# Performance work log

Measured on AMD Instinct MI355X. Metric: run time of the kernel, lower is better.

Reference implementation:

```python
import jax, jax.numpy as jnp
import numpy as np

N_NODES = 50000
N_EDGES = 800000
IN_DIM = 768
HID = 32
HEADS = 4
OUT_DIM = 128


def setup_inputs() -> dict:
    key = jax.random.key(0)
    ks = jax.random.split(key, 7)
    h = jax.random.normal(ks[0], (N_NODES, IN_DIM), dtype=jnp.float32)
    W1 = jax.random.normal(ks[1], (HEADS, IN_DIM, HID), dtype=jnp.float32) * (1.0 / np.sqrt(IN_DIM))
    a1 = jax.random.normal(ks[2], (HEADS, 2 * HID), dtype=jnp.float32) * (1.0 / np.sqrt(2 * HID))
    W2 = jax.random.normal(ks[3], (1, HEADS * HID, OUT_DIM), dtype=jnp.float32) * (1.0 / np.sqrt(HEADS * HID))
    a2 = jax.random.normal(ks[4], (1, 2 * OUT_DIM), dtype=jnp.float32) * (1.0 / np.sqrt(2 * OUT_DIM))
    src = jax.random.randint(ks[5], (N_EDGES,), 0, N_NODES, dtype=jnp.int32)
    dst = jax.random.randint(ks[6], (N_EDGES,), 0, N_NODES, dtype=jnp.int32)
    return {"h": h, "W1": W1, "a1": a1, "W2": W2, "a2": a2, "src": src, "dst": dst}


def gat_layer(h, W, a, src, dst, n_nodes):
    # W: [H, Din, D], a: [H, 2D]; returns concat of heads: [N, H*D]
    z = jnp.einsum('ni,hio->nho', h, W)          # [N, H, D]
    D = z.shape[-1]
    a_src, a_dst = a[:, :D], a[:, D:]
    s_src = jnp.einsum('nhd,hd->nh', z, a_src)   # [N, H]
    s_dst = jnp.einsum('nhd,hd->nh', z, a_dst)
    e = jax.nn.leaky_relu(s_src[src] + s_dst[dst], 0.01)  # [E, H]
    # edge softmax over incoming edges of each dst node
    e_max = jax.ops.segment_max(e, dst, num_segments=n_nodes)
    e_max = jnp.where(jnp.isfinite(e_max), e_max, 0.0)     # empty segments -> -inf
    ex = jnp.exp(e - e_max[dst])
    denom = jax.ops.segment_sum(ex, dst, num_segments=n_nodes)
    alpha = ex / jnp.maximum(denom[dst], 1e-9)             # [E, H]
    msg = alpha[:, :, None] * z[src]                       # [E, H, D]
    out = jax.ops.segment_sum(msg, dst, num_segments=n_nodes)  # [N, H, D]
    return out.reshape(n_nodes, -1)


def reference(h, W1, a1, W2, a2, src, dst):
    n = h.shape[0]
    h1 = jax.nn.elu(gat_layer(h, W1, a1, src, dst, n))   # [N, HEADS*HID]
    h2 = gat_layer(h1, W2, a2, src, dst, n)              # [N, OUT_DIM]
    return h2
```

## Files before the change

### kernel.cpp

```cpp
#include <hip/hip_runtime.h>

#define NN 50000
#define NE 800000
#define IND 768
#define CH  128
#define NBLK 196
#define GBM 64
#define GBK 32
#define MBLKS 782

typedef __attribute__((ext_vector_type(8))) short bf16x8;
typedef __attribute__((ext_vector_type(4))) float f32x4;

__device__ __forceinline__ unsigned short bf16_rne(float f) {
    unsigned u = __float_as_uint(f);
    u += 0x7fffu + ((u >> 16) & 1u);
    return (unsigned short)(u >> 16);
}
__device__ __forceinline__ float bf16_to_f(unsigned short b) {
    return __uint_as_float(((unsigned)b) << 16);
}

__global__ void prep_b1(const float* __restrict__ W1,
                        unsigned short* __restrict__ Bhi, unsigned short* __restrict__ Blo)
{
    int idx = blockIdx.x * blockDim.x + threadIdx.x;
    if (idx >= CH * IND) return;
    int n = idx / IND, k = idx % IND;
    float v = W1[(size_t)(n >> 5) * IND * 32 + (size_t)k * 32 + (n & 31)];
    int kt = k >> 5, kk = k & 31, j = kk >> 3, e = kk & 7;
    int g = n * 4 + (j ^ ((n >> 1) & 3));
    int off = kt * 4096 + g * 8 + e;
    unsigned short hi = bf16_rne(v);
    float lo = v - bf16_to_f(hi);
    Bhi[off] = hi;
    Blo[off] = bf16_rne(lo);
}

__global__ void prep_b2(const float* __restrict__ W2,
                        unsigned short* __restrict__ Bhi, unsigned short* __restrict__ Blo)
{
    int idx = blockIdx.x * blockDim.x + threadIdx.x;
    if (idx >= CH * CH) return;
    int n = idx / CH, k = idx % CH;
    float v = W2[(size_t)k * CH + n];
    int kt = k >> 5, kk = k & 31, j = kk >> 3, e = kk & 7;
    int g = n * 4 + (j ^ ((n >> 1) & 3));
    int off = kt * 4096 + g * 8 + e;
    unsigned short hi = bf16_rne(v);
    float lo = v - bf16_to_f(hi);
    Bhi[off] = hi;
    Blo[off] = bf16_rne(lo);
}

template<int H>
__global__ __launch_bounds__(256) void gemm_fused(
    const float* __restrict__ A,
    const unsigned short* __restrict__ Bthi, const unsigned short* __restrict__ Btlo,
    const float* __restrict__ av,
    unsigned short* __restrict__ Z16,
    float* __restrict__ ss, float* __restrict__ sd, int K)
{
    __shared__ unsigned short Ahi[2048];
    __shared__ unsigned short Alo[2048];
    __shared__ unsigned short Bs[2][4096];
    __shared__ float sred[2][64][2];

    const int t = threadIdx.x;
    const int lane = t & 63;
    const int w = t >> 6;
    const int wr = w >> 1, wc = w & 1;
    const int lrow = lane & 15, kg = lane >> 4;
    const int m0 = blockIdx.x * GBM;
    const int nt = K >> 5;

    const int ar = t >> 2, aj = t & 3;
    const bool avalid = (m0 + ar) < NN;
    const float* aptr = A + (size_t)(avalid ? (m0 + ar) : 0) * K + aj * 8;
    const int ag8 = (ar * 4 + (aj ^ ((ar >> 1) & 3))) * 8;

    int aoff[2];
    #pragma unroll
    for (int mi = 0; mi < 2; ++mi) {
        const int r = wr * 32 + mi * 16 + lrow;
        aoff[mi] = (r * 4 + (kg ^ ((r >> 1) & 3))) * 8;
    }
    int boff[4];
    #pragma unroll
    for (int ni = 0; ni < 4; ++ni) {
        const int n = wc * 64 + ni * 16 + lrow;
        boff[ni] = (n * 4 + (kg ^ ((n >> 1) & 3))) * 8;
    }

    f32x4 acc[2][4];
    #pragma unroll
    for (int i = 0; i < 2; ++i)
        #pragma unroll
        for (int j = 0; j < 4; ++j) acc[i][j] = (f32x4)(0.f);

    for (int kt = 0; kt < nt; ++kt) {
        float4 v0 = make_float4(0.f, 0.f, 0.f, 0.f);
        float4 v1 = make_float4(0.f, 0.f, 0.f, 0.f);
        if (avalid) {
            const float* p = aptr + kt * GBK;
            v0 = *(const float4*)p;
            v1 = *(const float4*)(p + 4);
        }
        float f[8] = {v0.x, v0.y, v0.z, v0.w, v1.x, v1.y, v1.z, v1.w};
        unsigned short hi[8], lo[8];
        #pragma unroll
        for (int q = 0; q < 8; ++q) {
            hi[q] = bf16_rne(f[q]);
            lo[q] = bf16_rne(f[q] - bf16_to_f(hi[q]));
        }
        __syncthreads();
        *(uint4*)&Ahi[ag8] = *(uint4*)hi;
        *(uint4*)&Alo[ag8] = *(uint4*)lo;
        #pragma unroll
        for (int i = 0; i < 4; ++i) {
            const int c = w * 4 + i;
            const int plane = c >> 3;
            const int co = (c & 7) * 512;
            const unsigned short* gs =
                (plane ? Btlo : Bthi) + (size_t)kt * 4096 + co + lane * 8;
            __builtin_amdgcn_global_load_lds(
                (const __attribute__((address_space(1))) unsigned int*)gs,
                (__attribute__((address_space(3))) unsigned int*)&Bs[plane][co],
                16, 0, 0);
        }
        __syncthreads();

        bf16x8 ahi[2], alo[2];
        #pragma unroll
        for (int mi = 0; mi < 2; ++mi) {
            ahi[mi] = *(const bf16x8*)&Ahi[aoff[mi]];
            alo[mi] = *(const bf16x8*)&Alo[aoff[mi]];
        }
        #pragma unroll
        for (int ni = 0; ni < 4; ++ni) {
            const bf16x8 bhi = *(const bf16x8*)&Bs[0][boff[ni]];
            const bf16x8 blo = *(const bf16x8*)&Bs[1][boff[ni]];
            #pragma unroll
            for (int mi = 0; mi < 2; ++mi) {
                acc[mi][ni] = __builtin_amdgcn_mfma_f32_16x16x32_bf16(ahi[mi], bhi, acc[mi][ni], 0, 0, 0);
                acc[mi][ni] = __builtin_amdgcn_mfma_f32_16x16x32_bf16(ahi[mi], blo, acc[mi][ni], 0, 0, 0);
                acc[mi][ni] = __builtin_amdgcn_mfma_f32_16x16x32_bf16(alo[mi], bhi, acc[mi][ni], 0, 0, 0);
            }
        }
    }

    const int NH = (H == 4) ? 2 : 1;
    float asc[4], adc[4];
    #pragma unroll
    for (int ni = 0; ni < 4; ++ni) {
        const int col = wc * 64 + ni * 16 + lrow;
        if (H == 4) {
            const int hh = col >> 5, d = col & 31;
            asc[ni] = av[hh * 64 + d];
            adc[ni] = av[hh * 64 + 32 + d];
        } else {
            asc[ni] = av[col];
            adc[ni] = av[128 + col];
        }
    }
    float es[2][4][2], ed[2][4][2];
    #pragma unroll
    for (int mi = 0; mi < 2; ++mi)
        #pragma unroll
        for (int j = 0; j < 4; ++j)
            #pragma unroll
            for (int q = 0; q < 2; ++q) { es[mi][j][q] = 0.f; ed[mi][j][q] = 0.f; }

    #pragma unroll
    for (int mi = 0; mi < 2; ++mi) {
        #pragma unroll
        for (int ni = 0; ni < 4; ++ni) {
            const int hh = (H == 4) ? (ni >> 1) : 0;
            const f32x4 a = acc[mi][ni];
            #pragma unroll
            for (int j = 0; j < 4; ++j) {
                es[mi][j][hh] = fmaf(a[j], asc[ni], es[mi][j][hh]);
                ed[mi][j][hh] = fmaf(a[j], adc[ni], ed[mi][j][hh]);
            }
        }
    }
    #pragma unroll
    for (int mi = 0; mi < 2; ++mi) {
        const int rbase = m0 + wr * 32 + mi * 16 + kg * 4;
        #pragma unroll
        for (int ni = 0; ni < 4; ++ni) {
            const int col = wc * 64 + ni * 16 + lrow;
            const f32x4 a = acc[mi][ni];
            #pragma unroll
            for (int j = 0; j < 4; ++j) {
                const int r = rbase + j;
                if (r < NN) Z16[(size_t)r * CH + col] = bf16_rne(a[j]);
            }
        }
    }
    #pragma unroll
    for (int off = 1; off < 16; off <<= 1) {
        #pragma unroll
        for (int mi = 0; mi < 2; ++mi)
            #pragma unroll
            for (int j = 0; j < 4; ++j)
                #pragma unroll
                for (int q = 0; q < NH; ++q) {
                    es[mi][j][q] += __shfl_xor(es[mi][j][q], off, 64);
                    ed[mi][j][q] += __shfl_xor(ed[mi][j][q], off, 64);
                }
    }
    if (H == 4) {
        if (lrow == 0) {
            #pragma unroll
            for (int mi = 0; mi < 2; ++mi)
                #pragma unroll
                for (int j = 0; j < 4; ++j) {
                    const int r = m0 + wr * 32 + mi * 16 + kg * 4 + j;
                    if (r < NN) {
                        #pragma unroll
                        for (int q = 0; q < 2; ++q) {
                            ss[r * 4 + wc * 2 + q] = es[mi][j][q];
                            sd[r * 4 + wc * 2 + q] = ed[mi][j][q];
                        }
                    }
                }
        }
    } else {
        if (lrow == 0) {
            #pragma unroll
            for (int mi = 0; mi < 2; ++mi)
                #pragma unroll
                for (int j = 0; j < 4; ++j) {
                    const int rl = wr * 32 + mi * 16 + kg * 4 + j;
                    sred[0][rl][wc] = es[mi][j][0];
                    sred[1][rl][wc] = ed[mi][j][0];
                }
        }
        __syncthreads();
        if (t < 64) {
            const int r = m0 + t;
            if (r < NN) {
                ss[r] = sred[0][t][0] + sred[0][t][1];
                sd[r] = sred[1][t][0] + sred[1][t][1];
            }
        }
    }
}

__global__ __launch_bounds__(256) void zero_cc(int* __restrict__ counts, int* __restrict__ cursor)
{
    int i = blockIdx.x * 256 + threadIdx.x;
    if (i < NN) { counts[i] = 0; cursor[i] = 0; }
}

__global__ void count_k(const int* __restrict__ dst, int* __restrict__ counts)
{
    int e = blockIdx.x * blockDim.x + threadIdx.x;
    if (e < NE) atomicAdd(&counts[dst[e]], 1);
}

__global__ __launch_bounds__(256) void scan1(const int* __restrict__ counts,
                                             int* __restrict__ exc, int* __restrict__ bsum)
{
    __shared__ int s[256];
    const int t = threadIdx.x;
    const int i = blockIdx.x * 256 + t;
    const int val = (i < NN) ? counts[i] : 0;
    s[t] = val;
    __syncthreads();
    #pragma unroll
    for (int off = 1; off < 256; off <<= 1) {
        int v = (t >= off) ? s[t - off] : 0;
        __syncthreads();
        s[t] += v;
        __syncthreads();
    }
    if (i < NN) exc[i] = s[t] - val;
    if (t == 255) bsum[blockIdx.x] = s[255];
}

__global__ __launch_bounds__(256) void scan2(const int* __restrict__ bsum,
                                             int* __restrict__ bexc)
{
    __shared__ int s[256];
    const int t = threadIdx.x;
    const int val = (t < NBLK) ? bsum[t] : 0;
    s[t] = val;
    __syncthreads();
    #pragma unroll
    for (int off = 1; off < 256; off <<= 1) {
        int v = (t >= off) ? s[t - off] : 0;
        __syncthreads();
        s[t] += v;
        __syncthreads();
    }
    bexc[t] = s[t] - val;
}

__global__ __launch_bounds__(256) void scan3(const int* __restrict__ exc,
                                             const int* __restrict__ bexc,
                                             int* __restrict__ offsets)
{
    const int i = blockIdx.x * 256 + threadIdx.x;
    if (i < NN) offsets[i] = exc[i] + bexc[i >> 8];
    if (i == 0) offsets[NN] = NE;
}

__global__ void scatter_es(const int* __restrict__ src, const int* __restrict__ dst,
                           const int* __restrict__ offsets, int* __restrict__ cursor,
                           int* __restrict__ es)
{
    int e = blockIdx.x * blockDim.x + threadIdx.x;
    if (e >= NE) return;
    int d = dst[e];
    int p = offsets[d] + atomicAdd(&cursor[d], 1);
    es[p] = src[e];
}

template<int H, bool ELU>
__global__ __launch_bounds__(256) void fused_agg(
    const int* __restrict__ offsets, const int* __restrict__ es,
    const float* __restrict__ s_src, const float* __restrict__ s_dst,
    const unsigned short* __restrict__ z16, float* __restrict__ out)
{
    const int wid = threadIdx.x >> 6;
    const int lane = threadIdx.x & 63;
    const int n = blockIdx.x * 4 + wid;
    const int beg = offsets[n], end = offsets[n + 1];
    const int deg = end - beg;

    __shared__ float alpha_sh[4][128][H];
    __shared__ int   es_sh[4][128];
    __shared__ int   maxdeg;
    if (threadIdx.x == 0) maxdeg = 0;
    __syncthreads();
    if (lane == 0) atomicMax(&maxdeg, deg);
    __syncthreads();
    const int nch = (maxdeg + 127) >> 7;

    float sdv[H];
    #pragma unroll
    for (int h = 0; h < H; ++h) sdv[h] = s_dst[(size_t)n * H + h];

    float m[H], ssum[H];
    #pragma unroll
    for (int h = 0; h < H; ++h) { m[h] = -INFINITY; ssum[h] = 0.f; }
    for (int i = beg + lane; i < end; i += 64) {
        const int s = es[i];
        if (H == 4) {
            const float4 sv = *(const float4*)&s_src[(size_t)s * 4];
            const float svv[4] = {sv.x, sv.y, sv.z, sv.w};
            #pragma unroll
            for (int h = 0; h < 4; ++h) {
                float v = svv[h] + sdv[h];
                v = v > 0.f ? v : 0.01f * v;
                const float mn = fmaxf(m[h], v);
                ssum[h] = ssum[h] * __expf(m[h] - mn) + __expf(v - mn);
                m[h] = mn;
            }
        } else {
            float v = s_src[s] + sdv[0];
            v = v > 0.f ? v : 0.01f * v;
            const float mn = fmaxf(m[0], v);
            ssum[0] = ssum[0] * __expf(m[0] - mn) + __expf(v - mn);
            m[0] = mn;
        }
    }
    float inv[H];
    #pragma unroll
    for (int h = 0; h < H; ++h) {
        float mg = m[h];
        #pragma unroll
        for (int off = 1; off < 64; off <<= 1)
            mg = fmaxf(mg, __shfl_xor(mg, off, 64));
        float sg = ssum[h] * __expf(m[h] - mg);
        #pragma unroll
        for (int off = 1; off < 64; off <<= 1)
            sg += __shfl_xor(sg, off, 64);
        m[h] = mg;
        inv[h] = 1.0f / fmaxf(sg, 1e-9f);
    }

    const int myh = (H == 4) ? (lane >> 4) : 0;
    float2 acc = make_float2(0.f, 0.f);
    for (int k = 0; k < nch; ++k) {
        const int base = beg + k * 128;
        int cnt = end - base;
        cnt = cnt < 0 ? 0 : (cnt > 128 ? 128 : cnt);
        for (int idx = lane; idx < cnt; idx += 64) {
            const int s = es[base + idx];
            es_sh[wid][idx] = s;
            if (H == 4) {
                const float4 sv = *(const float4*)&s_src[(size_t)s * 4];
                const float svv[4] = {sv.x, sv.y, sv.z, sv.w};
                float a4[4];
                #pragma unroll
                for (int h = 0; h < 4; ++h) {
                    float v = svv[h] + sdv[h];
                    v = v > 0.f ? v : 0.01f * v;
                    a4[h] = __expf(v - m[h]) * inv[h];
                }
                *(float4*)&alpha_sh[wid][idx][0] = make_float4(a4[0], a4[1], a4[2], a4[3]);
            } else {
                float v = s_src[s] + sdv[0];
                v = v > 0.f ? v : 0.01f * v;
                alpha_sh[wid][idx][0] = __expf(v - m[0]) * inv[0];
            }
        }
        __syncthreads();
        int j = 0;
        for (; j + 2 <= cnt; j += 2) {
            const int s0 = es_sh[wid][j],     s1 = es_sh[wid][j + 1];
            const float a0 = alpha_sh[wid][j][myh], a1 = alpha_sh[wid][j + 1][myh];
            const ushort2 u0 = *(const ushort2*)&z16[(size_t)s0 * CH + lane * 2];
            const ushort2 u1 = *(const ushort2*)&z16[(size_t)s1 * CH + lane * 2];
            acc.x = fmaf(a0, bf16_to_f(u0.x), acc.x); acc.y = fmaf(a0, bf16_to_f(u0.y), acc.y);
            acc.x = fmaf(a1, bf16_to_f(u1.x), acc.x); acc.y = fmaf(a1, bf16_to_f(u1.y), acc.y);
        }
        if (j < cnt) {
            const int s0 = es_sh[wid][j];
            const float a0 = alpha_sh[wid][j][myh];
            const ushort2 u0 = *(const ushort2*)&z16[(size_t)s0 * CH + lane * 2];
            acc.x = fmaf(a0, bf16_to_f(u0.x), acc.x); acc.y = fmaf(a0, bf16_to_f(u0.y), acc.y);
        }
        __syncthreads();
    }

    if (ELU) {
        acc.x = acc.x > 0.f ? acc.x : expm1f(acc.x);
        acc.y = acc.y > 0.f ? acc.y : expm1f(acc.y);
    }
    *(float2*)&out[(size_t)n * CH + lane * 2] = acc;
}

extern "C" void kernel_launch(void* const* d_in, const int* in_sizes, int n_in,
                              void* d_out, int out_size, void* d_ws, size_t ws_size,
                              hipStream_t stream)
{
    const float* h   = (const float*)d_in[0];
    const float* W1  = (const float*)d_in[1];
    const float* a1  = (const float*)d_in[2];
    const float* W2  = (const float*)d_in[3];
    const float* a2  = (const float*)d_in[4];
    const int*   src = (const int*)d_in[5];
    const int*   dst = (const int*)d_in[6];
    float* out = (float*)d_out;

    char* ws = (char*)d_ws;
    unsigned short* Bthi1 = (unsigned short*)(ws + 0);
    unsigned short* Btlo1 = (unsigned short*)(ws + 196608);
    unsigned short* Bthi2 = (unsigned short*)(ws + 393216);
    unsigned short* Btlo2 = (unsigned short*)(ws + 425984);
    float* ss      = (float*)(ws + 458752);
    float* sd      = (float*)(ws + 1258752);
    int*   counts  = (int*)  (ws + 2058752);
    int*   exc     = (int*)  (ws + 2258752);
    int*   bsum    = (int*)  (ws + 2458752);
    int*   bexc    = (int*)  (ws + 2459776);
    int*   offsets = (int*)  (ws + 2460800);
    int*   cursor  = (int*)  (ws + 2661056);
    int*   es      = (int*)  (ws + 2861056);
    unsigned short* z16 = (unsigned short*)(ws + 6061056);
    float* h1      = (float*)(ws + 18861056);

    const int EB = 256;
    const int egrid = (NE + EB - 1) / EB;
    const int sgrid = NN / 4;

    zero_cc<<<NBLK, 256, 0, stream>>>(counts, cursor);
    count_k<<<egrid, EB, 0, stream>>>(dst, counts);
    scan1<<<NBLK, 256, 0, stream>>>(counts, exc, bsum);
    scan2<<<1, 256, 0, stream>>>(bsum, bexc);
    scan3<<<NBLK, 256, 0, stream>>>(exc, bexc, offsets);
    scatter_es<<<egrid, EB, 0, stream>>>(src, dst, offsets, cursor, es);

    prep_b1<<<(CH * IND + 255) / 256, 256, 0, stream>>>(W1, Bthi1, Btlo1);
    prep_b2<<<(CH * CH + 255) / 256, 256, 0, stream>>>(W2, Bthi2, Btlo2);

    gemm_fused<4><<<MBLKS, 256, 0, stream>>>(h, Bthi1, Btlo1, a1, z16, ss, sd, IND);
    fused_agg<4, true><<<sgrid, 256, 0, stream>>>(offsets, es, ss, sd, z16, h1);

    gemm_fused<1><<<MBLKS, 256, 0, stream>>>(h1, Bthi2, Btlo2, a2, z16, ss, sd, CH);
    fused_agg<1, false><<<sgrid, 256, 0, stream>>>(offsets, es, ss, sd, z16, out);
}
```

Measured before the change: 269.9 us.

## Single-pass edge softmax for low-degree nodes and packed bf16 split conversion

In the aggregation kernel, nodes whose block max degree fits in one 128-edge chunk now read edge indices and source scores once. Raw logits are staged in shared memory while computing the online max and sum, then normalised in place. This avoids the second global gather of es and s_src and the block-wide syncs, and the gather loop is unrolled to four edges. The GEMM A-tile hi/lo bf16 split now uses v_cvt_pk_bf16_f32 inline asm instead of manual rounding. The fast path depends on each wave reading shared-memory entries written by other lanes of the same wave without a barrier, and the large-degree path remains as a fallback.

```diff
diff --git a/kernel.cpp b/kernel.cpp
--- a/kernel.cpp
+++ b/kernel.cpp
@@ -19,6 +19,31 @@
 }
 __device__ __forceinline__ float bf16_to_f(unsigned short b) {
     return __uint_as_float(((unsigned)b) << 16);
+}
+
+__device__ __forceinline__ void cvt_split_pk(const float4& u0, const float4& u1,
+                                             uint4& hi, uint4& lo)
+{
+    unsigned h0, h1, h2, h3;
+    asm("v_cvt_pk_bf16_f32 %0, %1, %2" : "=v"(h0) : "v"(u0.x), "v"(u0.y));
+    asm("v_cvt_pk_bf16_f32 %0, %1, %2" : "=v"(h1) : "v"(u0.z), "v"(u0.w));
+    asm("v_cvt_pk_bf16_f32 %0, %1, %2" : "=v"(h2) : "v"(u1.x), "v"(u1.y));
+    asm("v_cvt_pk_bf16_f32 %0, %1, %2" : "=v"(h3) : "v"(u1.z), "v"(u1.w));
+    const float l0 = u0.x - __uint_as_float(h0 << 16);
+    const float l1 = u0.y - __uint_as_float(h0 & 0xffff0000u);
+    const float l2 = u0.z - __uint_as_float(h1 << 16);
+    const float l3 = u0.w - __uint_as_float(h1 & 0xffff0000u);
+    const float l4 = u1.x - __uint_as_float(h2 << 16);
+    const float l5 = u1.y - __uint_as_float(h2 & 0xffff0000u);
+    const float l6 = u1.z - __uint_as_float(h3 << 16);
+    const float l7 = u1.w - __uint_as_float(h3 & 0xffff0000u);
+    unsigned g0, g1, g2, g3;
+    asm("v_cvt_pk_bf16_f32 %0, %1, %2" : "=v"(g0) : "v"(l0), "v"(l1));
+    asm("v_cvt_pk_bf16_f32 %0, %1, %2" : "=v"(g1) : "v"(l2), "v"(l3));
+    asm("v_cvt_pk_bf16_f32 %0, %1, %2" : "=v"(g2) : "v"(l4), "v"(l5));
+    asm("v_cvt_pk_bf16_f32 %0, %1, %2" : "=v"(g3) : "v"(l6), "v"(l7));
+    hi = make_uint4(h0, h1, h2, h3);
+    lo = make_uint4(g0, g1, g2, g3);
 }
 
 __global__ void prep_b1(const float* __restrict__ W1,
@@ -106,16 +131,11 @@
             v0 = *(const float4*)p;
             v1 = *(const float4*)(p + 4);
         }
-        float f[8] = {v0.x, v0.y, v0.z, v0.w, v1.x, v1.y, v1.z, v1.w};
-        unsigned short hi[8], lo[8];
-        #pragma unroll
-        for (int q = 0; q < 8; ++q) {
-            hi[q] = bf16_rne(f[q]);
-            lo[q] = bf16_rne(f[q] - bf16_to_f(hi[q]));
-        }
-        __syncthreads();
-        *(uint4*)&Ahi[ag8] = *(uint4*)hi;
-        *(uint4*)&Alo[ag8] = *(uint4*)lo;
+        uint4 hi, lo;
+        cvt_split_pk(v0, v1, hi, lo);
+        __syncthreads();
+        *(uint4*)&Ahi[ag8] = hi;
+        *(uint4*)&Alo[ag8] = lo;
         #pragma unroll
         for (int i = 0; i < 4; ++i) {
             const int c = w * 4 + i;
@@ -337,94 +357,153 @@
     __syncthreads();
     if (lane == 0) atomicMax(&maxdeg, deg);
     __syncthreads();
-    const int nch = (maxdeg + 127) >> 7;
 
     float sdv[H];
     #pragma unroll
     for (int h = 0; h < H; ++h) sdv[h] = s_dst[(size_t)n * H + h];
 
-    float m[H], ssum[H];
+    const int myh = (H == 4) ? (lane >> 4) : 0;
+    float m[H], ssum[H], inv[H];
     #pragma unroll
     for (int h = 0; h < H; ++h) { m[h] = -INFINITY; ssum[h] = 0.f; }
-    for (int i = beg + lane; i < end; i += 64) {
-        const int s = es[i];
-        if (H == 4) {
-            const float4 sv = *(const float4*)&s_src[(size_t)s * 4];
-            const float svv[4] = {sv.x, sv.y, sv.z, sv.w};
-            #pragma unroll
-            for (int h = 0; h < 4; ++h) {
-                float v = svv[h] + sdv[h];
-                v = v > 0.f ? v : 0.01f * v;
-                const float mn = fmaxf(m[h], v);
-                ssum[h] = ssum[h] * __expf(m[h] - mn) + __expf(v - mn);
-                m[h] = mn;
-            }
-        } else {
-            float v = s_src[s] + sdv[0];
-            v = v > 0.f ? v : 0.01f * v;
-            const float mn = fmaxf(m[0], v);
-            ssum[0] = ssum[0] * __expf(m[0] - mn) + __expf(v - mn);
-            m[0] = mn;
-        }
-    }
-    float inv[H];
-    #pragma unroll
-    for (int h = 0; h < H; ++h) {
-        float mg = m[h];
-        #pragma unroll
-        for (int off = 1; off < 64; off <<= 1)
-            mg = fmaxf(mg, __shfl_xor(mg, off, 64));
-        float sg = ssum[h] * __expf(m[h] - mg);
-        #pragma unroll
-        for (int off = 1; off < 64; off <<= 1)
-            sg += __shfl_xor(sg, off, 64);
-        m[h] = mg;
-        inv[h] = 1.0f / fmaxf(sg, 1e-9f);
-    }
-
-    const int myh = (H == 4) ? (lane >> 4) : 0;
     float2 acc = make_float2(0.f, 0.f);
-    for (int k = 0; k < nch; ++k) {
-        const int base = beg + k * 128;
-        int cnt = end - base;
-        cnt = cnt < 0 ? 0 : (cnt > 128 ? 128 : cnt);
-        for (int idx = lane; idx < cnt; idx += 64) {
-            const int s = es[base + idx];
+
+    if (maxdeg <= 128) {
+        for (int idx = lane; idx < deg; idx += 64) {
+            const int s = es[beg + idx];
             es_sh[wid][idx] = s;
             if (H == 4) {
                 const float4 sv = *(const float4*)&s_src[(size_t)s * 4];
                 const float svv[4] = {sv.x, sv.y, sv.z, sv.w};
-                float a4[4];
+                float v4[4];
                 #pragma unroll
                 for (int h = 0; h < 4; ++h) {
                     float v = svv[h] + sdv[h];
                     v = v > 0.f ? v : 0.01f * v;
-                    a4[h] = __expf(v - m[h]) * inv[h];
+                    v4[h] = v;
+                    const float mn = fmaxf(m[h], v);
+                    ssum[h] = ssum[h] * __expf(m[h] - mn) + __expf(v - mn);
+                    m[h] = mn;
                 }
-                *(float4*)&alpha_sh[wid][idx][0] = make_float4(a4[0], a4[1], a4[2], a4[3]);
+                *(float4*)&alpha_sh[wid][idx][0] = make_float4(v4[0], v4[1], v4[2], v4[3]);
             } else {
                 float v = s_src[s] + sdv[0];
                 v = v > 0.f ? v : 0.01f * v;
-                alpha_sh[wid][idx][0] = __expf(v - m[0]) * inv[0];
-            }
-        }
-        __syncthreads();
+                alpha_sh[wid][idx][0] = v;
+                const float mn = fmaxf(m[0], v);
+                ssum[0] = ssum[0] * __expf(m[0] - mn) + __expf(v - mn);
+                m[0] = mn;
+            }
+        }
+        #pragma unroll
+        for (int h = 0; h < H; ++h) {
+            float mg = m[h];
+            #pragma unroll
+            for (int off = 1; off < 64; off <<= 1)
+                mg = fmaxf(mg, __shfl_xor(mg, off, 64));
+            float sg = ssum[h] * __expf(m[h] - mg);
+            #pragma unroll
+            for (int off = 1; off < 64; off <<= 1)
+                sg += __shfl_xor(sg, off, 64);
+            m[h] = mg;
+            inv[h] = 1.0f / fmaxf(sg, 1e-9f);
+        }
+        for (int idx = lane; idx < deg; idx += 64) {
+            #pragma unroll
+            for (int h = 0; h < H; ++h)
+                alpha_sh[wid][idx][h] = __expf(alpha_sh[wid][idx][h] - m[h]) * inv[h];
+        }
         int j = 0;
-        for (; j + 2 <= cnt; j += 2) {
+        for (; j + 4 <= deg; j += 4) {
             const int s0 = es_sh[wid][j],     s1 = es_sh[wid][j + 1];
-            const float a0 = alpha_sh[wid][j][myh], a1 = alpha_sh[wid][j + 1][myh];
+            const int s2 = es_sh[wid][j + 2], s3 = es_sh[wid][j + 3];
+            const float a0 = alpha_sh[wid][j][myh],     a1 = alpha_sh[wid][j + 1][myh];
+            const float a2 = alpha_sh[wid][j + 2][myh], a3 = alpha_sh[wid][j + 3][myh];
             const ushort2 u0 = *(const ushort2*)&z16[(size_t)s0 * CH + lane * 2];
             const ushort2 u1 = *(const ushort2*)&z16[(size_t)s1 * CH + lane * 2];
+            const ushort2 u2 = *(const ushort2*)&z16[(size_t)s2 * CH + lane * 2];
+            const ushort2 u3 = *(const ushort2*)&z16[(size_t)s3 * CH + lane * 2];
             acc.x = fmaf(a0, bf16_to_f(u0.x), acc.x); acc.y = fmaf(a0, bf16_to_f(u0.y), acc.y);
             acc.x = fmaf(a1, bf16_to_f(u1.x), acc.x); acc.y = fmaf(a1, bf16_to_f(u1.y), acc.y);
-        }
-        if (j < cnt) {
+            acc.x = fmaf(a2, bf16_to_f(u2.x), acc.x); acc.y = fmaf(a2, bf16_to_f(u2.y), acc.y);
+            acc.x = fmaf(a3, bf16_to_f(u3.x), acc.x); acc.y = fmaf(a3, bf16_to_f(u3.y), acc.y);
+        }
+        for (; j < deg; ++j) {
             const int s0 = es_sh[wid][j];
             const float a0 = alpha_sh[wid][j][myh];
             const ushort2 u0 = *(const ushort2*)&z16[(size_t)s0 * CH + lane * 2];
             acc.x = fmaf(a0, bf16_to_f(u0.x), acc.x); acc.y = fmaf(a0, bf16_to_f(u0.y), acc.y);
         }
-        __syncthreads();
+    } else {
+        const int nch = (maxdeg + 127) >> 7;
+        for (int i = beg + lane; i < end; i += 64) {
+            const int s = es[i];
+            if (H == 4) {
+                const float4 sv = *(const float4*)&s_src[(size_t)s * 4];
+                const float svv[4] = {sv.x, sv.y, sv.z, sv.w};
+                #pragma unroll
+                for (int h = 0; h < 4; ++h) {
+                    float v = svv[h] + sdv[h];
+                    v = v > 0.f ? v : 0.01f * v;
+                    const float mn = fmaxf(m[h], v);
+                    ssum[h] = ssum[h] * __expf(m[h] - mn) + __expf(v - mn);
+                    m[h] = mn;
+                }
+            } else {
+                float v = s_src[s] + sdv[0];
+                v = v > 0.f ? v : 0.01f * v;
+                const float mn = fmaxf(m[0], v);
+                ssum[0] = ssum[0] * __expf(m[0] - mn) + __expf(v - mn);
+                m[0] = mn;
+            }
+        }
+        #pragma unroll
+        for (int h = 0; h < H; ++h) {
+            float mg = m[h];
+            #pragma unroll
+            for (int off = 1; off < 64; off <<= 1)
+                mg = fmaxf(mg, __shfl_xor(mg, off, 64));
+            float sg = ssum[h] * __expf(m[h] - mg);
+            #pragma unroll
+            for (int off = 1; off < 64; off <<= 1)
+                sg += __shfl_xor(sg, off, 64);
+            m[h] = mg;
+            inv[h] = 1.0f / fmaxf(sg, 1e-9f);
+        }
+        for (int k = 0; k < nch; ++k) {
+            const int base = beg + k * 128;
+            int cnt = end - base;
+            cnt = cnt < 0 ? 0 : (cnt > 128 ? 128 : cnt);
+            for (int idx = lane; idx < cnt; idx += 64) {
+                const int s = es[base + idx];
+                es_sh[wid][idx] = s;
+                if (H == 4) {
+                    const float4 sv = *(const float4*)&s_src[(size_t)s * 4];
+                    const float svv[4] = {sv.x, sv.y, sv.z, sv.w};
+                    float a4[4];
+                    #pragma unroll
+                    for (int h = 0; h < 4; ++h) {
+                        float v = svv[h] + sdv[h];
+                        v = v > 0.f ? v : 0.01f * v;
+                        a4[h] = __expf(v - m[h]) * inv[h];
+                    }
+                    *(float4*)&alpha_sh[wid][idx][0] = make_float4(a4[0], a4[1], a4[2], a4[3]);
+                } else {
+                    float v = s_src[s] + sdv[0];
+                    v = v > 0.f ? v : 0.01f * v;
+                    alpha_sh[wid][idx][0] = __expf(v - m[0]) * inv[0];
+                }
+            }
+            __syncthreads();
+            for (int j = 0; j < cnt; ++j) {
+                const int s0 = es_sh[wid][j];
+                const float a0 = alpha_sh[wid][j][myh];
+                const ushort2 u0 = *(const ushort2*)&z16[(size_t)s0 * CH + lane * 2];
+                acc.x = fmaf(a0, bf16_to_f(u0.x), acc.x);
+                acc.y = fmaf(a0, bf16_to_f(u0.y), acc.y);
+            }
+            __syncthreads();
+        }
     }
 
     if (ELU) {
```

Measured after the change: 245.3 us. 9.1% less time.
